# Kernel tuning notes

Hardware: AMD Instinct MI355X
Metric: run time of the kernel (lower is better)

## Reference

```python
import jax, jax.numpy as jnp
import numpy as np

EMBED_DIM = 1024
NUM_HEADS = 16
HEAD_DIM = EMBED_DIM // NUM_HEADS
B, S = 2, 2048


def setup_inputs() -> dict:
    key = jax.random.key(0)
    ks = jax.random.split(key, 10)
    inp = {
        "query": jax.random.normal(ks[0], (B, S, EMBED_DIM), dtype=jnp.float32),
        "key": jax.random.normal(ks[1], (B, S, EMBED_DIM), dtype=jnp.float32),
        "value": jax.random.normal(ks[2], (B, S, EMBED_DIM), dtype=jnp.float32),
        # 0 => masked key position (matches attn_mask == 0 in the torch code)
        "attn_mask": jax.random.randint(ks[3], (B, S), 0, 2, dtype=jnp.int32),
        "Wq": jax.random.normal(ks[4], (EMBED_DIM, EMBED_DIM), dtype=jnp.float32) * 0.02,
        "bq": jnp.zeros((EMBED_DIM,), dtype=jnp.float32),
        "Wk": jax.random.normal(ks[5], (EMBED_DIM, EMBED_DIM), dtype=jnp.float32) * 0.02,
        "bk": jnp.zeros((EMBED_DIM,), dtype=jnp.float32),
        "Wv": jax.random.normal(ks[6], (EMBED_DIM, EMBED_DIM), dtype=jnp.float32) * 0.02,
        "bv": jnp.zeros((EMBED_DIM,), dtype=jnp.float32),
    }
    return inp


def _proj_heads(x, W, b):
    # x: [B, S, E] -> [B, H, S, D]  (nn.Linear uses x @ W.T + b)
    y = x @ W.T + b
    Bx, Sx, E = y.shape
    return y.reshape(Bx, Sx, NUM_HEADS, HEAD_DIM).transpose(0, 2, 1, 3)


def reference(query, key, value, attn_mask, Wq, bq, Wk, bk, Wv, bv):
    q = _proj_heads(query, Wq, bq)   # [B,H,S,D]
    k = _proj_heads(key, Wk, bk)     # [B,H,S,D]
    v = _proj_heads(value, Wv, bv)   # [B,H,S,D]
    inv_scale = float(EMBED_DIM) ** 0.5  # NOTE: original divides by sqrt(embed_dim), not sqrt(head_dim)
    scores = jnp.einsum("bhqd,bhkd->bhqk", q, k) / inv_scale  # [B,H,S,S]
    mask = (attn_mask == 0)[:, None, None, :]  # [B,1,1,S] -> broadcast over [B,H,S,S]
    scores = jnp.where(mask, -jnp.inf, scores)
    attn = jax.nn.softmax(scores, axis=-1)
    # dropout omitted for deterministic reference (see notes)
    out = jnp.einsum("bhqk,bhkd->bhqd", attn, v)  # [B,H,S,D]
    return out
```

## Files before the change

### kernel.cpp

```cpp
#include <hip/hip_runtime.h>
#include <hip/hip_bf16.h>

constexpr int BB = 2;
constexpr int SS = 2048;
constexpr int EE = 1024;
constexpr int HH = 16;
constexpr int DD = 64;
constexpr int MM = BB * SS;
constexpr int CX = MM * EE;
constexpr int CW = EE * EE;
#define QSCALE 0.045084220027780106f

typedef __attribute__((ext_vector_type(8))) short short8;
typedef __attribute__((ext_vector_type(4))) float floatx4;
typedef __attribute__((ext_vector_type(4))) unsigned uintx4;

union fragu { uintx4 u; short8 s; };

__device__ inline short bf16bits(float x) {
    __hip_bfloat16 h = __float2bfloat16(x);
    return *reinterpret_cast<short*>(&h);
}

__device__ inline unsigned pkbf(float a, float b) {
    return (unsigned)(unsigned short)bf16bits(a) |
           ((unsigned)(unsigned short)bf16bits(b) << 16);
}

__device__ inline float fast_exp2(float x) {
#if __has_builtin(__builtin_amdgcn_exp2f)
    return __builtin_amdgcn_exp2f(x);
#else
    return exp2f(x);
#endif
}

__device__ inline void gl_lds16(const __hip_bfloat16* g, const short* l) {
    __builtin_amdgcn_global_load_lds(
        (const __attribute__((address_space(1))) void*)g,
        (__attribute__((address_space(3))) void*)l, 16, 0, 0);
}

__device__ inline int sigma_row(int p) {
    return (p & 0x23) | ((p & 0x0C) << 1) | ((p & 0x10) >> 2);
}

#define TURN4 { __asm__ volatile("s_waitcnt vmcnt(4)" ::: "memory"); __builtin_amdgcn_s_barrier(); }
#define TURN0 { __asm__ volatile("s_waitcnt vmcnt(0)" ::: "memory"); __builtin_amdgcn_s_barrier(); }

__global__ __launch_bounds__(256) void convert_kernel(
    const float* __restrict__ x0, const float* __restrict__ x1, const float* __restrict__ x2,
    const float* __restrict__ w0, const float* __restrict__ w1, const float* __restrict__ w2,
    __hip_bfloat16* __restrict__ xb, __hip_bfloat16* __restrict__ wb)
{
    const long long e = (long long)(blockIdx.x * 256 + threadIdx.x) * 8;
    const float* src;
    __hip_bfloat16* dst;
    if (e < 3LL * CX) {
        const int z = (int)(e >> 22);
        const int off = (int)(e & (CX - 1));
        src = ((z == 0) ? x0 : (z == 1) ? x1 : x2) + off;
        dst = xb + e;
    } else {
        const long long e2 = e - 3LL * CX;
        const int z = (int)(e2 >> 20);
        const int off = (int)(e2 & (CW - 1));
        src = ((z == 0) ? w0 : (z == 1) ? w1 : w2) + off;
        dst = wb + e2;
    }
    const float4 a = reinterpret_cast<const float4*>(src)[0];
    const float4 b = reinterpret_cast<const float4*>(src)[1];
    short8 r;
    r[0] = bf16bits(a.x); r[1] = bf16bits(a.y); r[2] = bf16bits(a.z); r[3] = bf16bits(a.w);
    r[4] = bf16bits(b.x); r[5] = bf16bits(b.y); r[6] = bf16bits(b.z); r[7] = bf16bits(b.w);
    *reinterpret_cast<short8*>(dst) = r;
}

__global__ __launch_bounds__(256) void proj_gemm(
    const __hip_bfloat16* __restrict__ xb,
    const __hip_bfloat16* __restrict__ wb,
    const float* __restrict__ bq, const float* __restrict__ bk, const float* __restrict__ bv,
    __hip_bfloat16* __restrict__ qws,
    __hip_bfloat16* __restrict__ kws,
    __hip_bfloat16* __restrict__ vtws)
{
    const int which = blockIdx.z;
    const __hip_bfloat16* A = xb + (size_t)which * CX;
    const __hip_bfloat16* W = wb + (size_t)which * CW;
    const float* bias = (which == 0) ? bq : (which == 1) ? bk : bv;

    const int m0   = blockIdx.x * 128;
    const int n0   = blockIdx.y * 128;
    const int tid  = threadIdx.x;
    const int wave = tid >> 6;
    const int lane = tid & 63;
    const int l15  = lane & 15;
    const int quad = lane >> 4;
    const int wr   = wave >> 1;
    const int wc   = wave & 1;

    __shared__ __align__(16) short As[128 * 32];
    __shared__ __align__(16) short Bs[128 * 32];

    const int dpos  = (lane & 7) ^ (lane >> 3);
    const int drloc = 2 * (lane >> 3) + (dpos >> 2);
    const int dgran = (dpos & 3) * 8;

    const int rbase = (l15 >> 1) * 64;
    const int rslot = (((l15 & 1) * 4 + quad) ^ (l15 >> 1)) * 8;

    floatx4 acc[4][4] = {};

    for (int k0 = 0; k0 < EE; k0 += 32) {
        __syncthreads();
        #pragma unroll
        for (int p = 0; p < 2; ++p) {
            const int rb16 = wave * 32 + p * 16;
            gl_lds16(A + (size_t)(m0 + rb16 + drloc) * EE + k0 + dgran, &As[rb16 * 32]);
            gl_lds16(W + (size_t)(n0 + rb16 + drloc) * EE + k0 + dgran, &Bs[rb16 * 32]);
        }
        __syncthreads();

        short8 af[4], bf[4];
        #pragma unroll
        for (int mt = 0; mt < 4; ++mt)
            af[mt] = *reinterpret_cast<const short8*>(
                &As[(wr * 32 + mt * 8) * 64 + rbase + rslot]);
        #pragma unroll
        for (int nt = 0; nt < 4; ++nt)
            bf[nt] = *reinterpret_cast<const short8*>(
                &Bs[(wc * 32 + nt * 8) * 64 + rbase + rslot]);

        #pragma unroll
        for (int mt = 0; mt < 4; ++mt)
            #pragma unroll
            for (int nt = 0; nt < 4; ++nt)
                acc[mt][nt] = __builtin_amdgcn_mfma_f32_16x16x32_bf16(af[mt], bf[nt], acc[mt][nt], 0, 0, 0);
    }

    #pragma unroll
    for (int nt = 0; nt < 4; ++nt) {
        const int n = n0 + wc * 64 + nt * 16 + l15;
        const float bval = bias[n];
        const int h = n >> 6, d = n & 63;
        #pragma unroll
        for (int mt = 0; mt < 4; ++mt) {
            #pragma unroll
            for (int r = 0; r < 4; ++r) {
                const int m = m0 + wr * 64 + mt * 16 + quad * 4 + r;
                const int b = m >> 11;
                const int s = m & (SS - 1);
                float val = acc[mt][nt][r] + bval;
                if (which == 0) val *= QSCALE;
                const __hip_bfloat16 hv = __float2bfloat16(val);
                if (which == 0)
                    qws[(((size_t)b * HH + h) * SS + s) * DD + d] = hv;
                else if (which == 1)
                    kws[(((size_t)b * HH + h) * SS + s) * DD + d] = hv;
                else
                    vtws[(((size_t)b * HH + h) * DD + d) * SS + s] = hv;
            }
        }
    }
}

#define ATTN_PF(NXT, T2) { \
    const int kn = (T2) * 64; \
    gl_lds16(K + (size_t)(kn + sk0) * DD + sg, &Ks[NXT][rb0 * 64]); \
    gl_lds16(VT + (size_t)(rb0 + srow) * SS + kn + sg, &Vs[NXT][rb0 * 64]); \
    gl_lds16(K + (size_t)(kn + sk1) * DD + sg, &Ks[NXT][rb1 * 64]); \
    gl_lds16(VT + (size_t)(rb1 + srow) * SS + kn + sg, &Vs[NXT][rb1 * 64]); }

#define ATTN_BODY(CUR, T) { \
    const int kt = (T) * 64; \
    floatx4 s0[4], s1[4]; \
    __builtin_amdgcn_s_setprio(1); \
    _Pragma("unroll") \
    for (int f = 0; f < 4; ++f) { \
        const int krow = (f * 16 + l15) * 64; \
        const short8 ka = *reinterpret_cast<const short8*>(&Ks[CUR][krow + (quad ^ swz) * 8]); \
        const short8 kb = *reinterpret_cast<const short8*>(&Ks[CUR][krow + ((quad + 4) ^ swz) * 8]); \
        floatx4 z = {}; \
        z = __builtin_amdgcn_mfma_f32_16x16x32_bf16(ka, qa0, z, 0, 0, 0); \
        z = __builtin_amdgcn_mfma_f32_16x16x32_bf16(kb, qa1, z, 0, 0, 0); \
        s0[f] = z; \
        floatx4 w = {}; \
        w = __builtin_amdgcn_mfma_f32_16x16x32_bf16(ka, qa2, w, 0, 0, 0); \
        w = __builtin_amdgcn_mfma_f32_16x16x32_bf16(kb, qa3, w, 0, 0, 0); \
        s1[f] = w; \
    } \
    __builtin_amdgcn_s_setprio(0); \
    fragu fa0, fa1, fb0, fb1; \
    _Pragma("unroll") \
    for (int f = 0; f < 4; ++f) { \
        const float4 mf = *reinterpret_cast<const float4*>( \
            &Ms[kt + 32 * (f >> 1) + 8 * quad + 4 * (f & 1)]); \
        const float e00 = fast_exp2(s0[f][0]) * mf.x; \
        const float e01 = fast_exp2(s0[f][1]) * mf.y; \
        const float e02 = fast_exp2(s0[f][2]) * mf.z; \
        const float e03 = fast_exp2(s0[f][3]) * mf.w; \
        const float e10 = fast_exp2(s1[f][0]) * mf.x; \
        const float e11 = fast_exp2(s1[f][1]) * mf.y; \
        const float e12 = fast_exp2(s1[f][2]) * mf.z; \
        const float e13 = fast_exp2(s1[f][3]) * mf.w; \
        uintx4& da = (f < 2) ? fa0.u : fa1.u; \
        uintx4& db = (f < 2) ? fb0.u : fb1.u; \
        const int i0 = (f & 1) * 2; \
        da[i0]     = pkbf(e00, e01); \
        da[i0 + 1] = pkbf(e02, e03); \
        db[i0]     = pkbf(e10, e11); \
        db[i0 + 1] = pkbf(e12, e13); \
    } \
    __builtin_amdgcn_s_setprio(1); \
    accl0 = __builtin_amdgcn_mfma_f32_16x16x32_bf16(fa0.s, ones, accl0, 0, 0, 0); \
    accl0 = __builtin_amdgcn_mfma_f32_16x16x32_bf16(fa1.s, ones, accl0, 0, 0, 0); \
    accl1 = __builtin_amdgcn_mfma_f32_16x16x32_bf16(fb0.s, ones, accl1, 0, 0, 0); \
    accl1 = __builtin_amdgcn_mfma_f32_16x16x32_bf16(fb1.s, ones, accl1, 0, 0, 0); \
    _Pragma("unroll") \
    for (int nt = 0; nt < 4; ++nt) { \
        const int vrow = (nt * 16 + l15) * 64; \
        const short8 vb0 = *reinterpret_cast<const short8*>(&Vs[CUR][vrow + (quad ^ swz) * 8]); \
        const short8 vb1 = *reinterpret_cast<const short8*>(&Vs[CUR][vrow + ((quad + 4) ^ swz) * 8]); \
        acc0[nt] = __builtin_amdgcn_mfma_f32_16x16x32_bf16(fa0.s, vb0, acc0[nt], 0, 0, 0); \
        acc0[nt] = __builtin_amdgcn_mfma_f32_16x16x32_bf16(fa1.s, vb1, acc0[nt], 0, 0, 0); \
        acc1[nt] = __builtin_amdgcn_mfma_f32_16x16x32_bf16(fb0.s, vb0, acc1[nt], 0, 0, 0); \
        acc1[nt] = __builtin_amdgcn_mfma_f32_16x16x32_bf16(fb1.s, vb1, acc1[nt], 0, 0, 0); \
    } \
    __builtin_amdgcn_s_setprio(0); }

__global__ __launch_bounds__(256) void attn_kernel(
    const __hip_bfloat16* __restrict__ qws,
    const __hip_bfloat16* __restrict__ kws,
    const __hip_bfloat16* __restrict__ vtws,
    const int* __restrict__ amask,
    float* __restrict__ out)
{
    const int flatb = blockIdx.y * gridDim.x + blockIdx.x;
    const int bh    = 4 * (flatb & 7) + ((flatb >> 3) & 3);
    const int b     = bh >> 4;
    const int q0    = (flatb >> 5) * 128;
    const int tid  = threadIdx.x;
    const int wave = tid >> 6;
    const int lane = tid & 63;
    const int l15  = lane & 15;
    const int quad = lane >> 4;

    const __hip_bfloat16* Q  = qws  + (size_t)bh * SS * DD;
    const __hip_bfloat16* K  = kws  + (size_t)bh * SS * DD;
    const __hip_bfloat16* VT = vtws + (size_t)bh * DD * SS;
    const int* msk = amask + b * SS;

    __shared__ __align__(16) short Ks[4][64 * 64];
    __shared__ __align__(16) short Vs[4][64 * 64];
    __shared__ __align__(16) float Ms[SS];

    #pragma unroll
    for (int i = 0; i < 2; ++i) {
        const int j = tid + i * 256;
        const int4 m4 = reinterpret_cast<const int4*>(msk)[j];
        float4 f4;
        f4.x = (float)m4.x; f4.y = (float)m4.y; f4.z = (float)m4.z; f4.w = (float)m4.w;
        reinterpret_cast<float4*>(Ms)[j] = f4;
    }

    const int qrow = q0 + wave * 32 + l15;
    const short8 qa0 = *reinterpret_cast<const short8*>(Q + (size_t)qrow * DD + quad * 8);
    const short8 qa1 = *reinterpret_cast<const short8*>(Q + (size_t)qrow * DD + 32 + quad * 8);
    const short8 qa2 = *reinterpret_cast<const short8*>(Q + (size_t)(qrow + 16) * DD + quad * 8);
    const short8 qa3 = *reinterpret_cast<const short8*>(Q + (size_t)(qrow + 16) * DD + 32 + quad * 8);

    const int swz = l15 & 7;

    short8 ones;
    #pragma unroll
    for (int i = 0; i < 8; ++i) ones[i] = (short)0x3F80;

    const int srow = lane >> 3;
    const int sg   = ((lane & 7) ^ srow) * 8;
    const int sk0  = sigma_row(wave * 16 + srow);
    const int sk1  = sigma_row(wave * 16 + 8 + srow);
    const int rb0  = wave * 16, rb1 = rb0 + 8;

    floatx4 acc0[4] = {}, acc1[4] = {};
    floatx4 accl0 = {}, accl1 = {};

    ATTN_PF(0, 0);
    ATTN_PF(1, 1);
    __asm__ volatile("s_waitcnt vmcnt(4) lgkmcnt(0)" ::: "memory");
    __builtin_amdgcn_s_barrier();

    for (int t = 0; t < 28; t += 4) {
        ATTN_PF(2, t + 2); ATTN_BODY(0, t);     TURN4;
        ATTN_PF(3, t + 3); ATTN_BODY(1, t + 1); TURN4;
        ATTN_PF(0, t + 4); ATTN_BODY(2, t + 2); TURN4;
        ATTN_PF(1, t + 5); ATTN_BODY(3, t + 3); TURN4;
    }
    ATTN_PF(2, 30); ATTN_BODY(0, 28); TURN4;
    ATTN_PF(3, 31); ATTN_BODY(1, 29); TURN4;
    ATTN_BODY(2, 30); TURN0;
    ATTN_BODY(3, 31);

    float i0[4], i1[4];
    #pragma unroll
    for (int r = 0; r < 4; ++r) {
        i0[r] = 1.f / accl0[r];
        i1[r] = 1.f / accl1[r];
    }

    const size_t obase = (size_t)bh * SS * DD;
    #pragma unroll
    for (int nt = 0; nt < 4; ++nt)
        #pragma unroll
        for (int r = 0; r < 4; ++r) {
            const int qq = q0 + wave * 32 + quad * 4 + r;
            const int d  = nt * 16 + l15;
            out[obase + (size_t)qq * DD + d] = acc0[nt][r] * i0[r];
            out[obase + (size_t)(qq + 16) * DD + d] = acc1[nt][r] * i1[r];
        }
}

extern "C" void kernel_launch(void* const* d_in, const int* in_sizes, int n_in,
                              void* d_out, int out_size, void* d_ws, size_t ws_size,
                              hipStream_t stream) {
    const float* q    = (const float*)d_in[0];
    const float* k    = (const float*)d_in[1];
    const float* v    = (const float*)d_in[2];
    const int*   mask = (const int*)d_in[3];
    const float* Wq   = (const float*)d_in[4];
    const float* bq   = (const float*)d_in[5];
    const float* Wk   = (const float*)d_in[6];
    const float* bk   = (const float*)d_in[7];
    const float* Wv   = (const float*)d_in[8];
    const float* bv   = (const float*)d_in[9];
    float* out = (float*)d_out;

    __hip_bfloat16* qws  = (__hip_bfloat16*)d_ws;
    __hip_bfloat16* kws  = qws + (size_t)CX;
    __hip_bfloat16* vtws = kws + (size_t)CX;
    __hip_bfloat16* xb   = vtws + (size_t)CX;
    __hip_bfloat16* wb   = xb + (size_t)3 * CX;

    const int cvt_blocks = (3 * CX + 3 * CW) / (256 * 8);
    convert_kernel<<<dim3(cvt_blocks), 256, 0, stream>>>(q, k, v, Wq, Wk, Wv, xb, wb);
    proj_gemm<<<dim3(MM / 128, EE / 128, 3), 256, 0, stream>>>(
        xb, wb, bq, bk, bv, qws, kws, vtws);
    attn_kernel<<<dim3(SS / 128, BB * HH), 256, 0, stream>>>(
        qws, kws, vtws, mask, out);
}
```

Before: 200.0 us.

## Split key range across wave halves with 64-row query tiles and LDS reduction

The attention kernel now uses 512-thread blocks covering 256 queries. Each wave owns 64 query rows and one half of the key sequence, and the two halves' partial outputs and row sums are combined through LDS at the end. The mask is folded in as an additive bias (0 or -1e30) used as the QK MFMA accumulator init, which removes the per-element multiply after exp. The aim is more reuse of each K/V tile per wave and fewer exp-path ops, at the cost of more registers, larger LDS use, half the grid size and an extra reduction step.

```diff
diff --git a/kernel.cpp b/kernel.cpp
--- a/kernel.cpp
+++ b/kernel.cpp
@@ -164,71 +164,65 @@
     }
 }
 
-#define ATTN_PF(NXT, T2) { \
-    const int kn = (T2) * 64; \
-    gl_lds16(K + (size_t)(kn + sk0) * DD + sg, &Ks[NXT][rb0 * 64]); \
-    gl_lds16(VT + (size_t)(rb0 + srow) * SS + kn + sg, &Vs[NXT][rb0 * 64]); \
-    gl_lds16(K + (size_t)(kn + sk1) * DD + sg, &Ks[NXT][rb1 * 64]); \
-    gl_lds16(VT + (size_t)(rb1 + srow) * SS + kn + sg, &Vs[NXT][rb1 * 64]); }
-
-#define ATTN_BODY(CUR, T) { \
+#define ATTN_PF(B, T) { \
+    const int kn = (T) * 64; \
+    gl_lds16(Kg + (size_t)(kn + sk0) * DD + sg, Ksg + (B) * 4096 + rb0 * 64); \
+    gl_lds16(VTg + (size_t)(rb0 + srow) * SS + kn + sg, Vsg + (B) * 4096 + rb0 * 64); \
+    gl_lds16(Kg + (size_t)(kn + sk1) * DD + sg, Ksg + (B) * 4096 + rb1 * 64); \
+    gl_lds16(VTg + (size_t)(rb1 + srow) * SS + kn + sg, Vsg + (B) * 4096 + rb1 * 64); }
+
+#define ATTN_BODY(B, T) { \
     const int kt = (T) * 64; \
-    floatx4 s0[4], s1[4]; \
+    floatx4 s[4][4]; \
     __builtin_amdgcn_s_setprio(1); \
     _Pragma("unroll") \
     for (int f = 0; f < 4; ++f) { \
         const int krow = (f * 16 + l15) * 64; \
-        const short8 ka = *reinterpret_cast<const short8*>(&Ks[CUR][krow + (quad ^ swz) * 8]); \
-        const short8 kb = *reinterpret_cast<const short8*>(&Ks[CUR][krow + ((quad + 4) ^ swz) * 8]); \
-        floatx4 z = {}; \
-        z = __builtin_amdgcn_mfma_f32_16x16x32_bf16(ka, qa0, z, 0, 0, 0); \
-        z = __builtin_amdgcn_mfma_f32_16x16x32_bf16(kb, qa1, z, 0, 0, 0); \
-        s0[f] = z; \
-        floatx4 w = {}; \
-        w = __builtin_amdgcn_mfma_f32_16x16x32_bf16(ka, qa2, w, 0, 0, 0); \
-        w = __builtin_amdgcn_mfma_f32_16x16x32_bf16(kb, qa3, w, 0, 0, 0); \
-        s1[f] = w; \
+        const short8 ka = *reinterpret_cast<const short8*>(Ksg + (B) * 4096 + krow + (quad ^ swz) * 8); \
+        const short8 kb = *reinterpret_cast<const short8*>(Ksg + (B) * 4096 + krow + ((quad + 4) ^ swz) * 8); \
+        const float4 mf = *reinterpret_cast<const float4*>( \
+            Msb + kt + 32 * (f >> 1) + 8 * quad + 4 * (f & 1)); \
+        floatx4 mb; mb[0] = mf.x; mb[1] = mf.y; mb[2] = mf.z; mb[3] = mf.w; \
+        _Pragma("unroll") \
+        for (int qb = 0; qb < 4; ++qb) { \
+            floatx4 z = __builtin_amdgcn_mfma_f32_16x16x32_bf16(ka, qa[qb][0], mb, 0, 0, 0); \
+            s[qb][f]  = __builtin_amdgcn_mfma_f32_16x16x32_bf16(kb, qa[qb][1], z, 0, 0, 0); \
+        } \
     } \
     __builtin_amdgcn_s_setprio(0); \
-    fragu fa0, fa1, fb0, fb1; \
+    fragu pk[4][2]; \
     _Pragma("unroll") \
-    for (int f = 0; f < 4; ++f) { \
-        const float4 mf = *reinterpret_cast<const float4*>( \
-            &Ms[kt + 32 * (f >> 1) + 8 * quad + 4 * (f & 1)]); \
-        const float e00 = fast_exp2(s0[f][0]) * mf.x; \
-        const float e01 = fast_exp2(s0[f][1]) * mf.y; \
-        const float e02 = fast_exp2(s0[f][2]) * mf.z; \
-        const float e03 = fast_exp2(s0[f][3]) * mf.w; \
-        const float e10 = fast_exp2(s1[f][0]) * mf.x; \
-        const float e11 = fast_exp2(s1[f][1]) * mf.y; \
-        const float e12 = fast_exp2(s1[f][2]) * mf.z; \
-        const float e13 = fast_exp2(s1[f][3]) * mf.w; \
-        uintx4& da = (f < 2) ? fa0.u : fa1.u; \
-        uintx4& db = (f < 2) ? fb0.u : fb1.u; \
-        const int i0 = (f & 1) * 2; \
-        da[i0]     = pkbf(e00, e01); \
-        da[i0 + 1] = pkbf(e02, e03); \
-        db[i0]     = pkbf(e10, e11); \
-        db[i0 + 1] = pkbf(e12, e13); \
+    for (int qb = 0; qb < 4; ++qb) \
+        _Pragma("unroll") \
+        for (int f = 0; f < 4; ++f) { \
+            const float e0 = fast_exp2(s[qb][f][0]); \
+            const float e1 = fast_exp2(s[qb][f][1]); \
+            const float e2 = fast_exp2(s[qb][f][2]); \
+            const float e3 = fast_exp2(s[qb][f][3]); \
+            const int i0 = (f & 1) * 2; \
+            pk[qb][f >> 1].u[i0]     = pkbf(e0, e1); \
+            pk[qb][f >> 1].u[i0 + 1] = pkbf(e2, e3); \
+        } \
+    __builtin_amdgcn_s_setprio(1); \
+    _Pragma("unroll") \
+    for (int qb = 0; qb < 4; ++qb) { \
+        accl[qb] = __builtin_amdgcn_mfma_f32_16x16x32_bf16(pk[qb][0].s, ones, accl[qb], 0, 0, 0); \
+        accl[qb] = __builtin_amdgcn_mfma_f32_16x16x32_bf16(pk[qb][1].s, ones, accl[qb], 0, 0, 0); \
     } \
-    __builtin_amdgcn_s_setprio(1); \
-    accl0 = __builtin_amdgcn_mfma_f32_16x16x32_bf16(fa0.s, ones, accl0, 0, 0, 0); \
-    accl0 = __builtin_amdgcn_mfma_f32_16x16x32_bf16(fa1.s, ones, accl0, 0, 0, 0); \
-    accl1 = __builtin_amdgcn_mfma_f32_16x16x32_bf16(fb0.s, ones, accl1, 0, 0, 0); \
-    accl1 = __builtin_amdgcn_mfma_f32_16x16x32_bf16(fb1.s, ones, accl1, 0, 0, 0); \
     _Pragma("unroll") \
     for (int nt = 0; nt < 4; ++nt) { \
         const int vrow = (nt * 16 + l15) * 64; \
-        const short8 vb0 = *reinterpret_cast<const short8*>(&Vs[CUR][vrow + (quad ^ swz) * 8]); \
-        const short8 vb1 = *reinterpret_cast<const short8*>(&Vs[CUR][vrow + ((quad + 4) ^ swz) * 8]); \
-        acc0[nt] = __builtin_amdgcn_mfma_f32_16x16x32_bf16(fa0.s, vb0, acc0[nt], 0, 0, 0); \
-        acc0[nt] = __builtin_amdgcn_mfma_f32_16x16x32_bf16(fa1.s, vb1, acc0[nt], 0, 0, 0); \
-        acc1[nt] = __builtin_amdgcn_mfma_f32_16x16x32_bf16(fb0.s, vb0, acc1[nt], 0, 0, 0); \
-        acc1[nt] = __builtin_amdgcn_mfma_f32_16x16x32_bf16(fb1.s, vb1, acc1[nt], 0, 0, 0); \
+        const short8 vb0 = *reinterpret_cast<const short8*>(Vsg + (B) * 4096 + vrow + (quad ^ swz) * 8); \
+        const short8 vb1 = *reinterpret_cast<const short8*>(Vsg + (B) * 4096 + vrow + ((quad + 4) ^ swz) * 8); \
+        _Pragma("unroll") \
+        for (int qb = 0; qb < 4; ++qb) { \
+            acc[qb][nt] = __builtin_amdgcn_mfma_f32_16x16x32_bf16(pk[qb][0].s, vb0, acc[qb][nt], 0, 0, 0); \
+            acc[qb][nt] = __builtin_amdgcn_mfma_f32_16x16x32_bf16(pk[qb][1].s, vb1, acc[qb][nt], 0, 0, 0); \
+        } \
     } \
     __builtin_amdgcn_s_setprio(0); }
 
-__global__ __launch_bounds__(256) void attn_kernel(
+__global__ __launch_bounds__(512, 2) void attn_kernel(
     const __hip_bfloat16* __restrict__ qws,
     const __hip_bfloat16* __restrict__ kws,
     const __hip_bfloat16* __restrict__ vtws,
@@ -238,36 +232,43 @@
     const int flatb = blockIdx.y * gridDim.x + blockIdx.x;
     const int bh    = 4 * (flatb & 7) + ((flatb >> 3) & 3);
     const int b     = bh >> 4;
-    const int q0    = (flatb >> 5) * 128;
+    const int q0    = (flatb >> 5) * 256;
     const int tid  = threadIdx.x;
     const int wave = tid >> 6;
     const int lane = tid & 63;
     const int l15  = lane & 15;
     const int quad = lane >> 4;
-
-    const __hip_bfloat16* Q  = qws  + (size_t)bh * SS * DD;
-    const __hip_bfloat16* K  = kws  + (size_t)bh * SS * DD;
-    const __hip_bfloat16* VT = vtws + (size_t)bh * DD * SS;
+    const int qg   = wave & 3;
+    const int kh   = wave >> 2;
+
+    const __hip_bfloat16* Q   = qws  + (size_t)bh * SS * DD;
+    const __hip_bfloat16* Kg  = kws  + (size_t)bh * SS * DD + (size_t)kh * 1024 * DD;
+    const __hip_bfloat16* VTg = vtws + (size_t)bh * DD * SS + (size_t)kh * 1024;
     const int* msk = amask + b * SS;
 
-    __shared__ __align__(16) short Ks[4][64 * 64];
-    __shared__ __align__(16) short Vs[4][64 * 64];
-    __shared__ __align__(16) float Ms[SS];
-
+    __shared__ __align__(16) short SM[16 * 4096 + 4096];
+    short* Ksg = &SM[kh * 4 * 4096];
+    short* Vsg = &SM[(8 + kh * 4) * 4096];
+    float* Msf = reinterpret_cast<float*>(&SM[16 * 4096]);
+    const float* Msb = Msf + kh * 1024;
+
+    {
+        const int4 m4 = reinterpret_cast<const int4*>(msk)[tid];
+        float4 f4;
+        f4.x = m4.x ? 0.f : -1e30f;
+        f4.y = m4.y ? 0.f : -1e30f;
+        f4.z = m4.z ? 0.f : -1e30f;
+        f4.w = m4.w ? 0.f : -1e30f;
+        reinterpret_cast<float4*>(Msf)[tid] = f4;
+    }
+
+    const int qrow = q0 + qg * 64 + l15;
+    short8 qa[4][2];
     #pragma unroll
-    for (int i = 0; i < 2; ++i) {
-        const int j = tid + i * 256;
-        const int4 m4 = reinterpret_cast<const int4*>(msk)[j];
-        float4 f4;
-        f4.x = (float)m4.x; f4.y = (float)m4.y; f4.z = (float)m4.z; f4.w = (float)m4.w;
-        reinterpret_cast<float4*>(Ms)[j] = f4;
-    }
-
-    const int qrow = q0 + wave * 32 + l15;
-    const short8 qa0 = *reinterpret_cast<const short8*>(Q + (size_t)qrow * DD + quad * 8);
-    const short8 qa1 = *reinterpret_cast<const short8*>(Q + (size_t)qrow * DD + 32 + quad * 8);
-    const short8 qa2 = *reinterpret_cast<const short8*>(Q + (size_t)(qrow + 16) * DD + quad * 8);
-    const short8 qa3 = *reinterpret_cast<const short8*>(Q + (size_t)(qrow + 16) * DD + 32 + quad * 8);
+    for (int qb = 0; qb < 4; ++qb) {
+        qa[qb][0] = *reinterpret_cast<const short8*>(Q + (size_t)(qrow + qb * 16) * DD + quad * 8);
+        qa[qb][1] = *reinterpret_cast<const short8*>(Q + (size_t)(qrow + qb * 16) * DD + 32 + quad * 8);
+    }
 
     const int swz = l15 & 7;
 
@@ -277,46 +278,70 @@
 
     const int srow = lane >> 3;
     const int sg   = ((lane & 7) ^ srow) * 8;
-    const int sk0  = sigma_row(wave * 16 + srow);
-    const int sk1  = sigma_row(wave * 16 + 8 + srow);
-    const int rb0  = wave * 16, rb1 = rb0 + 8;
-
-    floatx4 acc0[4] = {}, acc1[4] = {};
-    floatx4 accl0 = {}, accl1 = {};
+    const int rb0  = qg * 16, rb1 = rb0 + 8;
+    const int sk0  = sigma_row(rb0 + srow);
+    const int sk1  = sigma_row(rb1 + srow);
+
+    floatx4 acc[4][4] = {};
+    floatx4 accl[4] = {};
 
     ATTN_PF(0, 0);
     ATTN_PF(1, 1);
     __asm__ volatile("s_waitcnt vmcnt(4) lgkmcnt(0)" ::: "memory");
     __builtin_amdgcn_s_barrier();
 
-    for (int t = 0; t < 28; t += 4) {
+    for (int t = 0; t < 12; t += 4) {
         ATTN_PF(2, t + 2); ATTN_BODY(0, t);     TURN4;
         ATTN_PF(3, t + 3); ATTN_BODY(1, t + 1); TURN4;
         ATTN_PF(0, t + 4); ATTN_BODY(2, t + 2); TURN4;
         ATTN_PF(1, t + 5); ATTN_BODY(3, t + 3); TURN4;
     }
-    ATTN_PF(2, 30); ATTN_BODY(0, 28); TURN4;
-    ATTN_PF(3, 31); ATTN_BODY(1, 29); TURN4;
-    ATTN_BODY(2, 30); TURN0;
-    ATTN_BODY(3, 31);
-
-    float i0[4], i1[4];
-    #pragma unroll
-    for (int r = 0; r < 4; ++r) {
-        i0[r] = 1.f / accl0[r];
-        i1[r] = 1.f / accl1[r];
-    }
-
-    const size_t obase = (size_t)bh * SS * DD;
-    #pragma unroll
-    for (int nt = 0; nt < 4; ++nt)
-        #pragma unroll
-        for (int r = 0; r < 4; ++r) {
-            const int qq = q0 + wave * 32 + quad * 4 + r;
-            const int d  = nt * 16 + l15;
-            out[obase + (size_t)qq * DD + d] = acc0[nt][r] * i0[r];
-            out[obase + (size_t)(qq + 16) * DD + d] = acc1[nt][r] * i1[r];
+    ATTN_PF(2, 14); ATTN_BODY(0, 12); TURN4;
+    ATTN_PF(3, 15); ATTN_BODY(1, 13); TURN4;
+    ATTN_BODY(2, 14); TURN0;
+    ATTN_BODY(3, 15);
+
+    __syncthreads();
+    float* CB = reinterpret_cast<float*>(&SM[0]);
+    float* R  = CB + qg * 5120;
+    if (kh == 1) {
+        #pragma unroll
+        for (int qb = 0; qb < 4; ++qb)
+            #pragma unroll
+            for (int nt = 0; nt < 4; ++nt)
+                *reinterpret_cast<floatx4*>(R + ((qb * 4 + nt) * 64 + lane) * 4) = acc[qb][nt];
+        #pragma unroll
+        for (int qb = 0; qb < 4; ++qb)
+            *reinterpret_cast<floatx4*>(R + ((16 + qb) * 64 + lane) * 4) = accl[qb];
+    }
+    __syncthreads();
+    if (kh == 0) {
+        #pragma unroll
+        for (int qb = 0; qb < 4; ++qb)
+            #pragma unroll
+            for (int nt = 0; nt < 4; ++nt) {
+                const floatx4 p = *reinterpret_cast<const floatx4*>(R + ((qb * 4 + nt) * 64 + lane) * 4);
+                acc[qb][nt][0] += p[0]; acc[qb][nt][1] += p[1];
+                acc[qb][nt][2] += p[2]; acc[qb][nt][3] += p[3];
+            }
+        const size_t obase = (size_t)bh * SS * DD;
+        #pragma unroll
+        for (int qb = 0; qb < 4; ++qb) {
+            const floatx4 pl = *reinterpret_cast<const floatx4*>(R + ((16 + qb) * 64 + lane) * 4);
+            float inv[4];
+            #pragma unroll
+            for (int r = 0; r < 4; ++r)
+                inv[r] = 1.f / (accl[qb][r] + pl[r]);
+            #pragma unroll
+            for (int nt = 0; nt < 4; ++nt)
+                #pragma unroll
+                for (int r = 0; r < 4; ++r) {
+                    const int qq = q0 + qg * 64 + qb * 16 + quad * 4 + r;
+                    const int d  = nt * 16 + l15;
+                    out[obase + (size_t)qq * DD + d] = acc[qb][nt][r] * inv[r];
+                }
         }
+    }
 }
 
 extern "C" void kernel_launch(void* const* d_in, const int* in_sizes, int n_in,
@@ -344,6 +369,6 @@
     convert_kernel<<<dim3(cvt_blocks), 256, 0, stream>>>(q, k, v, Wq, Wk, Wv, xb, wb);
     proj_gemm<<<dim3(MM / 128, EE / 128, 3), 256, 0, stream>>>(
         xb, wb, bq, bk, bv, qws, kws, vtws);
-    attn_kernel<<<dim3(SS / 128, BB * HH), 256, 0, stream>>>(
+    attn_kernel<<<dim3(SS / 256, BB * HH), 512, 0, stream>>>(
         qws, kws, vtws, mask, out);
 }
```

Result: faster. 196.1 us, median of 2 (-2.0%).
